# Kernel optimization log

Measured on AMD Instinct MI355X. Metric: run time of the kernel, lower is better.

Reference implementation:

```python
import jax, jax.numpy as jnp
import numpy as np

B, T, H, M = 16, 1024, 512, 80
NHEADS, HDIM = 8, H // 8


def _p(key, shape, scale=0.05):
    return scale * jax.random.normal(key, shape, dtype=jnp.float32)


def setup_inputs() -> dict:
    key = jax.random.key(0)
    ks = jax.random.split(key, 20)
    return {
        "encoder_memory": jax.random.normal(ks[0], (B, T, H), dtype=jnp.float32),
        "target_mel": jax.random.normal(ks[1], (B, T, M), dtype=jnp.float32),
        # prenet Linear(mel_dim -> hidden_dim)
        "w_prenet": _p(ks[2], (H, M)), "b_prenet": _p(ks[3], (H,)),
        # MultiheadAttention packed in-proj (3H, H) and out-proj (H, H)
        "in_proj_w": _p(ks[4], (3 * H, H)), "in_proj_b": _p(ks[5], (3 * H,)),
        "out_proj_w": _p(ks[6], (H, H)), "out_proj_b": _p(ks[7], (H,)),
        # 2-layer LSTM (torch gate order i,f,g,o); h0=c0=0 each step so W_hh acts on zeros
        "w_ih0": _p(ks[8], (4 * H, 2 * H)), "w_hh0": _p(ks[9], (4 * H, H)),
        "b_ih0": _p(ks[10], (4 * H,)), "b_hh0": _p(ks[11], (4 * H,)),
        "w_ih1": _p(ks[12], (4 * H, H)), "w_hh1": _p(ks[13], (4 * H, H)),
        "b_ih1": _p(ks[14], (4 * H,)), "b_hh1": _p(ks[15], (4 * H,)),
        # mel projection Linear(hidden_dim -> mel_dim)
        "w_mel": _p(ks[16], (M, H)), "b_mel": _p(ks[17], (M,)),
    }


def _lstm_cell_zero_state(x, w_ih, w_hh, b_ih, b_hh):
    # single step from zero (h, c): the W_hh @ h0 term is exactly zero
    gates = x @ w_ih.T + (b_ih + b_hh)  # (B,T,4H)
    i, f, g, o = jnp.split(gates, 4, axis=-1)
    c = jax.nn.sigmoid(i) * jnp.tanh(g)  # f * c_prev == 0
    return jax.nn.sigmoid(o) * jnp.tanh(c)


def reference(encoder_memory, target_mel, w_prenet, b_prenet,
              in_proj_w, in_proj_b, out_proj_w, out_proj_b,
              w_ih0, w_hh0, b_ih0, b_hh0, w_ih1, w_hh1, b_ih1, b_hh1,
              w_mel, b_mel):
    # teacher forcing: prev_mel at step t is zeros (t=0) else target_mel[:, t-1]
    prev = jnp.concatenate(
        [jnp.zeros((B, 1, M), dtype=target_mel.dtype), target_mel[:, :-1]], axis=1)
    pre = jax.nn.relu(prev @ w_prenet.T + b_prenet)  # (B,T,H); dropout is identity (eval)

    # cross-attention: each step's length-1 query attends over all encoder frames,
    # which vectorizes to standard (no-mask) MHA with queries = pre
    wq, wk, wv = jnp.split(in_proj_w, 3, axis=0)
    bq, bk, bv = jnp.split(in_proj_b, 3, axis=0)
    q = (pre @ wq.T + bq).reshape(B, T, NHEADS, HDIM)
    k = (encoder_memory @ wk.T + bk).reshape(B, T, NHEADS, HDIM)
    v = (encoder_memory @ wv.T + bv).reshape(B, T, NHEADS, HDIM)
    scale = 1.0 / jnp.sqrt(jnp.float32(HDIM))
    scores = jnp.einsum('bqhd,bkhd->bhqk', q * scale, k)  # (B,8,T,T)
    attn = jax.nn.softmax(scores, axis=-1)
    ctx = jnp.einsum('bhqk,bkhd->bqhd', attn, v).reshape(B, T, H)
    attn_out = ctx @ out_proj_w.T + out_proj_b  # (B,T,H)

    dec_in = jnp.concatenate([pre, attn_out], axis=-1)  # (B,T,2H)
    h1 = _lstm_cell_zero_state(dec_in, w_ih0, w_hh0, b_ih0, b_hh0)
    h2 = _lstm_cell_zero_state(h1, w_ih1, w_hh1, b_ih1, b_hh1)
    return h2 @ w_mel.T + b_mel  # (B,T,M)
```

## Files before the change

kernel.cpp:

```cpp
#include <hip/hip_runtime.h>


typedef _Float16 f16;
typedef _Float16 f16x8 __attribute__((ext_vector_type(8)));
typedef _Float16 f16x4 __attribute__((ext_vector_type(4)));
typedef float f32x4 __attribute__((ext_vector_type(4)));

constexpr int B_ = 16, T_ = 1024, H_ = 512, M_ = 80;
constexpr int NH_ = 8, D_ = 64;
constexpr int N_ = B_ * T_;

#define MFMA16(a, b, c) __builtin_amdgcn_mfma_f32_16x16x32_f16(a, b, c, 0, 0, 0)

__device__ __forceinline__ void gload_lds16(const f16* g, f16* l) {
  __builtin_amdgcn_global_load_lds(
      (const __attribute__((address_space(1))) void*)g,
      (__attribute__((address_space(3))) void*)l, 16, 0, 0);
}

template <int EPI, bool CONCATA, bool NCHK>
__global__ __launch_bounds__(256) void mgemm(
    const f16* __restrict__ A, const f16* __restrict__ A2,
    const f16* __restrict__ Wt, const float* __restrict__ bias,
    const float* __restrict__ bias2, float scale, void* __restrict__ outp,
    int K, int N) {
  __shared__ f16 As[128 * 64];
  __shared__ f16 Bs[128 * 64];
  const int tid = threadIdx.x;
  const int lane = tid & 63, wid = tid >> 6;
  const int lq = lane & 15, lg = lane >> 4;
  const int wm = wid >> 1, wn = wid & 1;
  const int r0 = blockIdx.x * 128, c0 = blockIdx.y * 128;

  f32x4 acc[4][4] = {};

  for (int k0 = 0; k0 < K; k0 += 64) {
#pragma unroll
    for (int it = 0; it < 4; ++it) {
      const int off = it * 4096 + wid * 1024 + lane * 16;
      const int row = off >> 7;
      const int cb = (off >> 4) & 7;
      const int kc = k0 + ((cb ^ (row & 7)) << 3);
      const f16* src;
      if (CONCATA) {
        src = (kc < 512) ? (A + (size_t)(r0 + row) * 512 + kc)
                         : (A2 + (size_t)(r0 + row) * 512 + (kc - 512));
      } else {
        src = A + (size_t)(r0 + row) * K + kc;
      }
      gload_lds16(src, (f16*)((char*)As + off));
    }
#pragma unroll
    for (int it = 0; it < 4; ++it) {
      const int off = it * 4096 + wid * 1024 + lane * 16;
      const int row = off >> 7;
      const int cb = (off >> 4) & 7;
      int crow = c0 + row;
      if (NCHK) crow = crow < N ? crow : N - 1;
      gload_lds16(Wt + (size_t)crow * K + k0 + ((cb ^ (row & 7)) << 3),
                  (f16*)((char*)Bs + off));
    }
    __syncthreads();
#pragma unroll
    for (int kk = 0; kk < 2; ++kk) {
      f16x8 af[4], bf[4];
#pragma unroll
      for (int m = 0; m < 4; ++m) {
        const int row = wm * 64 + m * 16 + lq;
        af[m] = *(const f16x8*)((const char*)As + row * 128 +
                                (((kk * 4 + lg) ^ (row & 7)) << 4));
      }
#pragma unroll
      for (int n = 0; n < 4; ++n) {
        const int row = wn * 64 + n * 16 + lq;
        bf[n] = *(const f16x8*)((const char*)Bs + row * 128 +
                                (((kk * 4 + lg) ^ (row & 7)) << 4));
      }
#pragma unroll
      for (int m = 0; m < 4; ++m)
#pragma unroll
        for (int n = 0; n < 4; ++n) acc[m][n] = MFMA16(af[m], bf[n], acc[m][n]);
    }
    __syncthreads();
  }

#pragma unroll
  for (int m = 0; m < 4; ++m) {
    const int rbase = r0 + wm * 64 + m * 16 + lg * 4;
#pragma unroll
    for (int n = 0; n < 4; ++n) {
      const int col = c0 + wn * 64 + n * 16 + lq;
      if (NCHK && col >= N) continue;
      const float bsum = bias[col] + (bias2 ? bias2[col] : 0.f);
      const f32x4 a = acc[m][n];
      if (EPI == 3) {
        const int b = rbase >> 10, t = rbase & (T_ - 1);
        const int head = col >> 6, d = col & 63;
        f16x4 pk;
#pragma unroll
        for (int r = 0; r < 4; ++r) pk[r] = (f16)((a[r] + bsum) * scale);
        *(f16x4*)((f16*)outp + ((size_t)((b * NH_ + head) * D_ + d)) * T_ + t) =
            pk;
      } else {
#pragma unroll
        for (int r = 0; r < 4; ++r) {
          const int row = rbase + r;
          float v = (a[r] + bsum) * scale;
          if (EPI == 1) v = fmaxf(v, 0.f);
          if (EPI == 4)
            ((float*)outp)[(size_t)row * N + col] = v;
          else
            ((f16*)outp)[(size_t)row * N + col] = (f16)v;
        }
      }
    }
  }
}

template <bool CONCATA>
__global__ __launch_bounds__(256, 2) void lstm_fused(
    const f16* __restrict__ A, const f16* __restrict__ A2,
    const f16* __restrict__ Wih, const float* __restrict__ bih,
    const float* __restrict__ bhh, f16* __restrict__ Hout_) {
  constexpr int K = CONCATA ? 1024 : 512;
  __shared__ f16 As[128 * 64];
  __shared__ f16 Bs[3][128 * 64];
  const int tid = threadIdx.x;
  const int lane = tid & 63, wid = tid >> 6;
  const int lq = lane & 15, lg = lane >> 4;
  const int wm = wid >> 1, wn = wid & 1;
  const int r0 = blockIdx.x * 128, c0 = blockIdx.y * 128;

  f32x4 acc[3][4][4] = {};

  for (int k0 = 0; k0 < K; k0 += 64) {
#pragma unroll
    for (int it = 0; it < 4; ++it) {
      const int off = it * 4096 + tid * 16;
      const int row = off >> 7;
      const int cb = (off >> 4) & 7;
      const int kc = k0 + ((cb ^ (row & 7)) << 3);
      const f16* src;
      if (CONCATA) {
        src = (kc < 512) ? (A + (size_t)(r0 + row) * 512 + kc)
                         : (A2 + (size_t)(r0 + row) * 512 + (kc - 512));
      } else {
        src = A + (size_t)(r0 + row) * K + kc;
      }
      gload_lds16(src, (f16*)((char*)As + off));
    }
#pragma unroll
    for (int g = 0; g < 3; ++g) {
      const int gbase = (g == 0) ? 0 : 512 * (g + 1);
#pragma unroll
      for (int it = 0; it < 4; ++it) {
        const int off = it * 4096 + tid * 16;
        const int row = off >> 7;
        const int cb = (off >> 4) & 7;
        gload_lds16(
            Wih + (size_t)(gbase + c0 + row) * K + k0 + ((cb ^ (row & 7)) << 3),
            (f16*)((char*)&Bs[g][0] + off));
      }
    }
    __syncthreads();
#pragma unroll
    for (int kk = 0; kk < 2; ++kk) {
      f16x8 af[4];
#pragma unroll
      for (int m = 0; m < 4; ++m) {
        const int row = wm * 64 + m * 16 + lq;
        af[m] = *(const f16x8*)((const char*)As + row * 128 +
                                (((kk * 4 + lg) ^ (row & 7)) << 4));
      }
#pragma unroll
      for (int g = 0; g < 3; ++g)
#pragma unroll
        for (int n = 0; n < 4; ++n) {
          const int row = wn * 64 + n * 16 + lq;
          const f16x8 bf = *(const f16x8*)((const char*)&Bs[g][0] + row * 128 +
                                           (((kk * 4 + lg) ^ (row & 7)) << 4));
#pragma unroll
          for (int m = 0; m < 4; ++m)
            acc[g][m][n] = MFMA16(af[m], bf, acc[g][m][n]);
        }
    }
    __syncthreads();
  }

#pragma unroll
  for (int n = 0; n < 4; ++n) {
    const int c = c0 + wn * 64 + n * 16 + lq;
    const float bi = bih[c] + bhh[c];
    const float bg = bih[1024 + c] + bhh[1024 + c];
    const float bo = bih[1536 + c] + bhh[1536 + c];
#pragma unroll
    for (int m = 0; m < 4; ++m) {
      const int rbase = r0 + wm * 64 + m * 16 + lg * 4;
#pragma unroll
      for (int r = 0; r < 4; ++r) {
        const float gi = acc[0][m][n][r] + bi;
        const float gg = acc[1][m][n][r] + bg;
        const float go = acc[2][m][n][r] + bo;
        const float si = 1.f / (1.f + __expf(-gi));
        const float so = 1.f / (1.f + __expf(-go));
        const float tg = 2.f / (1.f + __expf(-2.f * gg)) - 1.f;
        const float cc = si * tg;
        const float tc = 2.f / (1.f + __expf(-2.f * cc)) - 1.f;
        Hout_[(size_t)(rbase + r) * 512 + c] = (f16)(so * tc);
      }
    }
  }
}

__global__ __launch_bounds__(256, 2) void kv_fused(
    const f16* __restrict__ A, const f16* __restrict__ Wt,
    const float* __restrict__ bias, f16* __restrict__ kout,
    f16* __restrict__ vout) {
  constexpr int K = 512;
  __shared__ f16 As[128 * 64];
  __shared__ f16 Bs[2][128 * 64];
  const int tid = threadIdx.x;
  const int lane = tid & 63, wid = tid >> 6;
  const int lq = lane & 15, lg = lane >> 4;
  const int wm = wid >> 1, wn = wid & 1;
  const int r0 = blockIdx.x * 128, c0 = blockIdx.y * 128;

  f32x4 acc[2][4][4] = {};

  for (int k0 = 0; k0 < K; k0 += 64) {
#pragma unroll
    for (int it = 0; it < 4; ++it) {
      const int off = it * 4096 + tid * 16;
      const int row = off >> 7;
      const int cb = (off >> 4) & 7;
      const int kc = k0 + ((cb ^ (row & 7)) << 3);
      gload_lds16(A + (size_t)(r0 + row) * K + kc, (f16*)((char*)As + off));
    }
#pragma unroll
    for (int g = 0; g < 2; ++g) {
#pragma unroll
      for (int it = 0; it < 4; ++it) {
        const int off = it * 4096 + tid * 16;
        const int row = off >> 7;
        const int cb = (off >> 4) & 7;
        gload_lds16(
            Wt + (size_t)(g * 512 + c0 + row) * K + k0 + ((cb ^ (row & 7)) << 3),
            (f16*)((char*)&Bs[g][0] + off));
      }
    }
    __syncthreads();
#pragma unroll
    for (int kk = 0; kk < 2; ++kk) {
      f16x8 af[4];
#pragma unroll
      for (int m = 0; m < 4; ++m) {
        const int row = wm * 64 + m * 16 + lq;
        af[m] = *(const f16x8*)((const char*)As + row * 128 +
                                (((kk * 4 + lg) ^ (row & 7)) << 4));
      }
#pragma unroll
      for (int g = 0; g < 2; ++g)
#pragma unroll
        for (int n = 0; n < 4; ++n) {
          const int row = wn * 64 + n * 16 + lq;
          const f16x8 bf = *(const f16x8*)((const char*)&Bs[g][0] + row * 128 +
                                           (((kk * 4 + lg) ^ (row & 7)) << 4));
#pragma unroll
          for (int m = 0; m < 4; ++m)
            acc[g][m][n] = MFMA16(af[m], bf, acc[g][m][n]);
        }
    }
    __syncthreads();
  }

#pragma unroll
  for (int m = 0; m < 4; ++m) {
    const int rbase = r0 + wm * 64 + m * 16 + lg * 4;
    const int b = rbase >> 10, t = rbase & (T_ - 1);
#pragma unroll
    for (int n = 0; n < 4; ++n) {
      const int col = c0 + wn * 64 + n * 16 + lq;
      const float bk = bias[col];
#pragma unroll
      for (int r = 0; r < 4; ++r)
        kout[(size_t)(rbase + r) * 512 + col] = (f16)(acc[0][m][n][r] + bk);
      const float bv = bias[512 + col];
      const int head = col >> 6, d = col & 63;
      f16x4 pk;
#pragma unroll
      for (int r = 0; r < 4; ++r) pk[r] = (f16)(acc[1][m][n][r] + bv);
      *(f16x4*)(vout + ((size_t)((b * NH_ + head) * D_ + d)) * T_ + t) = pk;
    }
  }
}

__global__ __launch_bounds__(256) void attn_mfma4(
    const f16* __restrict__ q, const f16* __restrict__ k,
    const f16* __restrict__ vT, f16* __restrict__ ctx) {
  __shared__ f16 Ks[2][64 * 64];
  __shared__ f16 Vs[2][64 * 64];
  __shared__ f16 Ps[4][16 * 64];
  const int bid = blockIdx.x;
  const int wq = (bid & 7) * 64 + (bid >> 3);
  const int qt = wq & 3, bh = wq >> 2;
  const int head = bh & 7, b = bh >> 3;
  const int tid = threadIdx.x, lane = tid & 63, wid = tid >> 6;
  const int lq = lane & 15, lg = lane >> 4;

  const f16* kbase = k + ((size_t)b * T_) * H_ + head * D_;
  const f16* vbase = vT + (size_t)bh * D_ * T_;

  auto stage = [&](int kt, int buf) {
#pragma unroll
    for (int it = 0; it < 2; ++it) {
      const int off = it * 4096 + tid * 16;
      const int row = off >> 7;
      const int sc = ((((off >> 4) & 7) ^ (row & 7)) << 3);
      gload_lds16(kbase + (size_t)(kt * 64 + row) * H_ + sc,
                  (f16*)((char*)&Ks[buf][0] + off));
      gload_lds16(vbase + (size_t)row * T_ + kt * 64 + sc,
                  (f16*)((char*)&Vs[buf][0] + off));
    }
  };

  const int q0 = qt * 256 + wid * 64;
  f16x8 qf[4][2];
#pragma unroll
  for (int s = 0; s < 4; ++s)
#pragma unroll
    for (int kk = 0; kk < 2; ++kk)
      qf[s][kk] = *(const f16x8*)(q + ((size_t)(b * T_) + q0 + s * 16 + lq) * H_ +
                                  head * D_ + kk * 32 + lg * 8);

  float m_run[4] = {-1e30f, -1e30f, -1e30f, -1e30f};
  float l_run[4] = {0.f, 0.f, 0.f, 0.f};
  f32x4 accO[4][4] = {};
  char* pw = (char*)&Ps[wid][0] + lq * 128;
  const int psw = (lq & 7) << 4;

  stage(0, 0);
  __syncthreads();

  for (int kt = 0; kt < T_ / 64; ++kt) {
    const int cur = kt & 1;
    if (kt < T_ / 64 - 1) stage(kt + 1, cur ^ 1);

    f16x8 kf[4][2], vf[4][2];
#pragma unroll
    for (int n = 0; n < 4; ++n)
#pragma unroll
      for (int kk = 0; kk < 2; ++kk) {
        const int row = n * 16 + lq;
        kf[n][kk] = *(const f16x8*)((const char*)&Ks[cur][0] + row * 128 +
                                    (((kk * 4 + lg) ^ (row & 7)) << 4));
        vf[n][kk] = *(const f16x8*)((const char*)&Vs[cur][0] + row * 128 +
                                    (((kk * 4 + lg) ^ (row & 7)) << 4));
      }

#pragma unroll
    for (int s = 0; s < 4; ++s) {
      f32x4 ssw[4] = {};
      __builtin_amdgcn_s_setprio(1);
#pragma unroll
      for (int n = 0; n < 4; ++n)
#pragma unroll
        for (int kk = 0; kk < 2; ++kk)
          ssw[n] = MFMA16(kf[n][kk], qf[s][kk], ssw[n]);
      __builtin_amdgcn_s_setprio(0);

      float mloc = -1e30f;
#pragma unroll
      for (int n = 0; n < 4; ++n)
#pragma unroll
        for (int r = 0; r < 4; ++r) mloc = fmaxf(mloc, ssw[n][r]);
      mloc = fmaxf(mloc, __shfl_xor(mloc, 16, 64));
      mloc = fmaxf(mloc, __shfl_xor(mloc, 32, 64));

      const bool noresc = __all(mloc - m_run[s] <= 8.f);
      if (!noresc) {
        const float nm = fmaxf(m_run[s], mloc);
        const float corr = exp2f(m_run[s] - nm);
        m_run[s] = nm;
        l_run[s] *= corr;
#pragma unroll
        for (int n = 0; n < 4; ++n) {
          accO[s][n][0] *= corr; accO[s][n][1] *= corr;
          accO[s][n][2] *= corr; accO[s][n][3] *= corr;
        }
      }
      float sl = 0.f;
#pragma unroll
      for (int n = 0; n < 4; ++n) {
        f16x4 pk;
#pragma unroll
        for (int r = 0; r < 4; ++r) {
          const float p = exp2f(ssw[n][r] - m_run[s]);
          sl += p;
          pk[r] = (f16)p;
        }
        *(f16x4*)(pw + ((n * 32 + lg * 8) ^ psw)) = pk;
      }
      sl += __shfl_xor(sl, 16, 64);
      sl += __shfl_xor(sl, 32, 64);
      l_run[s] += sl;

      f16x8 pb[2];
#pragma unroll
      for (int kk = 0; kk < 2; ++kk)
        pb[kk] = *(const f16x8*)(pw + ((((kk * 4 + lg) << 4)) ^ psw));
      __builtin_amdgcn_s_setprio(1);
#pragma unroll
      for (int n = 0; n < 4; ++n)
#pragma unroll
        for (int kk = 0; kk < 2; ++kk)
          accO[s][n] = MFMA16(vf[n][kk], pb[kk], accO[s][n]);
      __builtin_amdgcn_s_setprio(0);
    }
    __syncthreads();
  }

#pragma unroll
  for (int s = 0; s < 4; ++s) {
    const float inv = 1.f / l_run[s];
    const size_t rowoff = ((size_t)(b * T_) + q0 + s * 16 + lq) * H_ + head * D_;
#pragma unroll
    for (int n = 0; n < 4; ++n) {
      f16x4 o;
#pragma unroll
      for (int r = 0; r < 4; ++r) o[r] = (f16)(accO[s][n][r] * inv);
      *(f16x4*)(ctx + rowoff + n * 16 + lg * 4) = o;
    }
  }
}

constexpr int C0 = 2097152;
constexpr int C1 = C0 + 196608;
constexpr int C2 = C1 + 65536;
constexpr int C3 = C2 + 524288;
constexpr int C4 = C3 + 262144;
constexpr int C5 = C4 + 10240;
constexpr int C6 = C5 + 524288;
constexpr int C7 = C6 + 16384;
__global__ void conv_all(const float* __restrict__ enc, const float* __restrict__ inw,
                         const float* __restrict__ outw, const float* __restrict__ wih0,
                         const float* __restrict__ wih1, const float* __restrict__ wmel,
                         const float* __restrict__ tmel, const float* __restrict__ wpre,
                         f16* denc, f16* dinw, f16* doutw, f16* dwih0,
                         f16* dwih1, f16* dwmel, f16* dpm, f16* dwp) {
  const int i = blockIdx.x * blockDim.x + threadIdx.x;
  if (i >= C7) return;
  if (i < C5) {
    const float* s;
    f16* d;
    int off;
    if (i < C0) { s = enc; d = denc; off = i; }
    else if (i < C1) { s = inw; d = dinw; off = i - C0; }
    else if (i < C2) { s = outw; d = doutw; off = i - C1; }
    else if (i < C3) { s = wih0; d = dwih0; off = i - C2; }
    else if (i < C4) { s = wih1; d = dwih1; off = i - C3; }
    else { s = wmel; d = dwmel; off = i - C4; }
    const float4 v = ((const float4*)s)[off];
    f16x4 o = {(f16)v.x, (f16)v.y, (f16)v.z, (f16)v.w};
    ((f16x4*)d)[off] = o;
  } else if (i < C6) {
    const int j = i - C5;
    const int r = j >> 5, c4 = (j & 31) * 4;
    const int t = r & (T_ - 1);
    f16x4 o = {};
    if (t != 0 && c4 < M_) {
      const float4 v = *(const float4*)(tmel + (size_t)(r - 1) * M_ + c4);
      o = {(f16)v.x, (f16)v.y, (f16)v.z, (f16)v.w};
    }
    *(f16x4*)(dpm + (size_t)r * 128 + c4) = o;
  } else {
    const int j = i - C6;
    const int r = j >> 5, c4 = (j & 31) * 4;
    f16x4 o = {};
    if (c4 < M_) {
      const float4 v = *(const float4*)(wpre + (size_t)r * M_ + c4);
      o = {(f16)v.x, (f16)v.y, (f16)v.z, (f16)v.w};
    }
    *(f16x4*)(dwp + (size_t)r * 128 + c4) = o;
  }
}

extern "C" void kernel_launch(void* const* d_in, const int* in_sizes, int n_in,
                              void* d_out, int out_size, void* d_ws,
                              size_t ws_size, hipStream_t stream) {
  const float* enc = (const float*)d_in[0];
  const float* tmel = (const float*)d_in[1];
  const float* w_pre = (const float*)d_in[2];
  const float* b_pre = (const float*)d_in[3];
  const float* inw = (const float*)d_in[4];
  const float* inb = (const float*)d_in[5];
  const float* outw = (const float*)d_in[6];
  const float* outb = (const float*)d_in[7];
  const float* wih0 = (const float*)d_in[8];
  const float* bih0 = (const float*)d_in[10];
  const float* bhh0 = (const float*)d_in[11];
  const float* wih1 = (const float*)d_in[12];
  const float* bih1 = (const float*)d_in[14];
  const float* bhh1 = (const float*)d_in[15];
  const float* wmel = (const float*)d_in[16];
  const float* bmel = (const float*)d_in[17];

  f16* wsh = (f16*)d_ws;
  const size_t SEG = (size_t)N_ * H_;
  f16* EncB = wsh;
  f16* h1 = wsh + SEG;
  f16* pre = wsh + 2 * SEG;
  f16* qb = wsh + 3 * SEG;
  f16* kbuf = wsh + 4 * SEG;
  f16* vTb = wsh + 5 * SEG;
  f16* ctx = wsh + 6 * SEG;
  f16* aout = EncB;
  f16* h2 = qb;
  f16* WP = wsh + 7 * SEG;
  f16* WIN = WP + 512 * 128;
  f16* WOUT = WIN + 1536 * 512;
  f16* WIH0 = WOUT + 512 * 512;
  f16* WIH1 = WIH0 + 2048 * 1024;
  f16* WMEL = WIH1 + 2048 * 512;
  f16* PM = WMEL + 80 * 512;

  const dim3 blk(256);
  conv_all<<<(C7 + 255) / 256, blk, 0, stream>>>(
      enc, inw, outw, wih0, wih1, wmel, tmel, w_pre, EncB, WIN, WOUT, WIH0,
      WIH1, WMEL, PM, WP);

  const dim3 g512(N_ / 128, 4), g80(N_ / 128, 1);
  mgemm<1, false, false><<<g512, blk, 0, stream>>>(PM, nullptr, WP, b_pre,
                                                   nullptr, 1.f, pre, 128, 512);
  mgemm<0, false, false><<<g512, blk, 0, stream>>>(
      pre, nullptr, WIN, inb, nullptr, 0.125f * 1.44269504088896f, qb, 512, 512);
  kv_fused<<<g512, blk, 0, stream>>>(EncB, WIN + 512 * 512, inb + 512, kbuf,
                                     vTb);
  attn_mfma4<<<dim3(512), blk, 0, stream>>>(qb, kbuf, vTb, ctx);
  mgemm<0, false, false><<<g512, blk, 0, stream>>>(ctx, nullptr, WOUT, outb,
                                                   nullptr, 1.f, aout, 512, 512);
  lstm_fused<true><<<g512, blk, 0, stream>>>(pre, aout, WIH0, bih0, bhh0, h1);
  lstm_fused<false><<<g512, blk, 0, stream>>>(h1, nullptr, WIH1, bih1, bhh1, h2);
  mgemm<4, false, true><<<g80, blk, 0, stream>>>(h2, nullptr, WMEL, bmel,
                                                 nullptr, 1.f, (float*)d_out,
                                                 512, 80);
}
```

Measured before the change: 316.8 us.

## Halve attention query tile per block and batch QK MFMAs before softmax

The attention kernel now gives each block 128 queries (32 per wave) instead of 256, doubling the grid to 1024 blocks for better occupancy and CU fill on the device. Within each key tile, all QK^T MFMAs for both query sub-tiles are issued together before V fragments are loaded, which lowers register pressure and lets the softmax of one sub-tile overlap the MFMAs of the other. In exchange, K/V tiles are streamed from global memory twice as many times overall, and the per-block K/V staging cost is amortized over fewer queries.

Result: faster. 288.6 us (-8.9%).

```diff
diff --git a/kernel.cpp b/kernel.cpp
--- a/kernel.cpp
+++ b/kernel.cpp
@@ -294,15 +294,15 @@
   }
 }
 
-__global__ __launch_bounds__(256) void attn_mfma4(
+__global__ __launch_bounds__(256) void attn_mfma5(
     const f16* __restrict__ q, const f16* __restrict__ k,
     const f16* __restrict__ vT, f16* __restrict__ ctx) {
   __shared__ f16 Ks[2][64 * 64];
   __shared__ f16 Vs[2][64 * 64];
   __shared__ f16 Ps[4][16 * 64];
   const int bid = blockIdx.x;
-  const int wq = (bid & 7) * 64 + (bid >> 3);
-  const int qt = wq & 3, bh = wq >> 2;
+  const int nid = (bid & 7) * 128 + (bid >> 3);
+  const int qt = nid & 7, bh = nid >> 3;
   const int head = bh & 7, b = bh >> 3;
   const int tid = threadIdx.x, lane = tid & 63, wid = tid >> 6;
   const int lq = lane & 15, lg = lane >> 4;
@@ -323,18 +323,17 @@
     }
   };
 
-  const int q0 = qt * 256 + wid * 64;
-  f16x8 qf[4][2];
-#pragma unroll
-  for (int s = 0; s < 4; ++s)
+  const int q0 = qt * 128 + wid * 32;
+  f16x8 qf[2][2];
+#pragma unroll
+  for (int s = 0; s < 2; ++s)
 #pragma unroll
     for (int kk = 0; kk < 2; ++kk)
       qf[s][kk] = *(const f16x8*)(q + ((size_t)(b * T_) + q0 + s * 16 + lq) * H_ +
                                   head * D_ + kk * 32 + lg * 8);
 
-  float m_run[4] = {-1e30f, -1e30f, -1e30f, -1e30f};
-  float l_run[4] = {0.f, 0.f, 0.f, 0.f};
-  f32x4 accO[4][4] = {};
+  float m_run[2] = {-1e30f, -1e30f}, l_run[2] = {0.f, 0.f};
+  f32x4 accO[2][4] = {};
   char* pw = (char*)&Ps[wid][0] + lq * 128;
   const int psw = (lq & 7) << 4;
 
@@ -345,7 +344,7 @@
     const int cur = kt & 1;
     if (kt < T_ / 64 - 1) stage(kt + 1, cur ^ 1);
 
-    f16x8 kf[4][2], vf[4][2];
+    f16x8 kf[4][2];
 #pragma unroll
     for (int n = 0; n < 4; ++n)
 #pragma unroll
@@ -353,26 +352,35 @@
         const int row = n * 16 + lq;
         kf[n][kk] = *(const f16x8*)((const char*)&Ks[cur][0] + row * 128 +
                                     (((kk * 4 + lg) ^ (row & 7)) << 4));
+      }
+    f32x4 ssw[2][4] = {};
+    __builtin_amdgcn_s_setprio(1);
+#pragma unroll
+    for (int s = 0; s < 2; ++s)
+#pragma unroll
+      for (int n = 0; n < 4; ++n)
+#pragma unroll
+        for (int kk = 0; kk < 2; ++kk)
+          ssw[s][n] = MFMA16(kf[n][kk], qf[s][kk], ssw[s][n]);
+    __builtin_amdgcn_s_setprio(0);
+
+    f16x8 vf[4][2];
+#pragma unroll
+    for (int n = 0; n < 4; ++n)
+#pragma unroll
+      for (int kk = 0; kk < 2; ++kk) {
+        const int row = n * 16 + lq;
         vf[n][kk] = *(const f16x8*)((const char*)&Vs[cur][0] + row * 128 +
                                     (((kk * 4 + lg) ^ (row & 7)) << 4));
       }
 
 #pragma unroll
-    for (int s = 0; s < 4; ++s) {
-      f32x4 ssw[4] = {};
-      __builtin_amdgcn_s_setprio(1);
+    for (int s = 0; s < 2; ++s) {
+      float mloc = -1e30f;
 #pragma unroll
       for (int n = 0; n < 4; ++n)
 #pragma unroll
-        for (int kk = 0; kk < 2; ++kk)
-          ssw[n] = MFMA16(kf[n][kk], qf[s][kk], ssw[n]);
-      __builtin_amdgcn_s_setprio(0);
-
-      float mloc = -1e30f;
-#pragma unroll
-      for (int n = 0; n < 4; ++n)
-#pragma unroll
-        for (int r = 0; r < 4; ++r) mloc = fmaxf(mloc, ssw[n][r]);
+        for (int r = 0; r < 4; ++r) mloc = fmaxf(mloc, ssw[s][n][r]);
       mloc = fmaxf(mloc, __shfl_xor(mloc, 16, 64));
       mloc = fmaxf(mloc, __shfl_xor(mloc, 32, 64));
 
@@ -394,7 +402,7 @@
         f16x4 pk;
 #pragma unroll
         for (int r = 0; r < 4; ++r) {
-          const float p = exp2f(ssw[n][r] - m_run[s]);
+          const float p = exp2f(ssw[s][n][r] - m_run[s]);
           sl += p;
           pk[r] = (f16)p;
         }
@@ -420,7 +428,7 @@
   }
 
 #pragma unroll
-  for (int s = 0; s < 4; ++s) {
+  for (int s = 0; s < 2; ++s) {
     const float inv = 1.f / l_run[s];
     const size_t rowoff = ((size_t)(b * T_) + q0 + s * 16 + lq) * H_ + head * D_;
 #pragma unroll
@@ -535,7 +543,7 @@
       pre, nullptr, WIN, inb, nullptr, 0.125f * 1.44269504088896f, qb, 512, 512);
   kv_fused<<<g512, blk, 0, stream>>>(EncB, WIN + 512 * 512, inb + 512, kbuf,
                                      vTb);
-  attn_mfma4<<<dim3(512), blk, 0, stream>>>(qb, kbuf, vTb, ctx);
+  attn_mfma5<<<dim3(1024), blk, 0, stream>>>(qb, kbuf, vTb, ctx);
   mgemm<0, false, false><<<g512, blk, 0, stream>>>(ctx, nullptr, WOUT, outb,
                                                    nullptr, 1.f, aout, 512, 512);
   lstm_fused<true><<<g512, blk, 0, stream>>>(pre, aout, WIH0, bih0, bhh0, h1);
```
